# Kernel optimization log

Measured on AMD Instinct MI355X. Metric: run time of the kernel, lower is better.

Reference implementation:

```python
import jax, jax.numpy as jnp
import numpy as np

V = 1024      # visible_size (channel_size)
H = 2048      # hidden_size
F = V + H     # full_size
T = 64        # timesteps
REC = 0.8     # params['lambda']


def setup_inputs() -> dict:
    key = jax.random.key(0)
    k1, k2, k3 = jax.random.split(key, 3)
    X = jax.random.normal(k1, (T, V), jnp.float32)
    # scale W so tanh does not fully saturate (fan-in scaling, like default init)
    W = jax.random.normal(k2, (F, F), jnp.float32) / np.float32(np.sqrt(F))
    b = jax.random.normal(k3, (F,), jnp.float32) * 0.01
    # Lambda: visible block = REC, hidden block = 1, diagonal of visible block = 1
    lam = jnp.concatenate(
        [jnp.full((V, V), REC, jnp.float32), jnp.ones((V, H), jnp.float32)], axis=1
    )
    lam = lam.at[jnp.arange(V), jnp.arange(V)].set(1.0)
    return {"X": X, "W": W, "b": b, "lam": lam}


def reference(X, W, b, lam):
    v = lam.shape[0]           # visible size
    one_minus_lam_vis = 1.0 - lam[:, :v]  # zero outside visible block anyway

    def step(carry, x_t):
        R, _ = carry
        WR = R @ W.T + b                      # [V, F] Linear applied row-wise
        U = lam * WR                          # gated recurrent part
        # I has x_t broadcast across rows in the visible block, zeros elsewhere
        U = U.at[:, :v].add(one_minus_lam_vis * x_t[None, :])
        R_next = jnp.tanh(U)                  # phi = torch.tanh
        return (R_next, U), None

    R0 = jnp.zeros((v, W.shape[0]), X.dtype)
    (_, U_last), _ = jax.lax.scan(step, (R0, R0), X)
    # torch.diag(U[:, :visible]) -> diagonal entries, shape [V]
    idx = jnp.arange(v)
    return U_last[idx, idx]
```

## Files before the change

### kernel.cpp

```cpp
#include <hip/hip_runtime.h>
#include <math.h>

#define V 1024
#define H 2048
#define F 3072
#define T 64
#define REC 0.8f

#define BM 64
#define BN 96
#define KT16 (F / 16)
#define NSS  (KT16 / 4)


typedef _Float16 half8 __attribute__((ext_vector_type(8)));
typedef float floatx16 __attribute__((ext_vector_type(16)));

__device__ __forceinline__ void gld16(const void* g, void* l) {
    __builtin_amdgcn_global_load_lds(
        (const __attribute__((address_space(1))) void*)g,
        (__attribute__((address_space(3))) void*)l, 16, 0, 0);
}

__device__ __forceinline__ float fast_tanh(float u) {
    float e = __expf(2.f * u);
    return 1.f - 2.f * __builtin_amdgcn_rcpf(e + 1.f);
}

__global__ __launch_bounds__(256)
void conv_w_fm(const float* __restrict__ W, _Float16* __restrict__ Wfm) {
    const int ct = blockIdx.y;
    const int ix = blockIdx.x * 256 + threadIdx.x;
    const int kt = ix / 192;
    const int q  = ix % 192;
    const int n  = ct * 96 + ((q >> 6) & 3) * 32 + (q & 31);
    const int k0 = kt * 16 + ((q >> 5) & 1) * 8;
    const float* src = W + (size_t)n * F + k0;
    float4 v0 = *(const float4*)src;
    float4 v1 = *(const float4*)(src + 4);
    half8 o = { (_Float16)v0.x, (_Float16)v0.y, (_Float16)v0.z, (_Float16)v0.w,
                (_Float16)v1.x, (_Float16)v1.y, (_Float16)v1.z, (_Float16)v1.w };
    *(half8*)(Wfm + ((size_t)(ct * KT16 + kt) * 1536 + q * 8)) = o;
}

__global__ __launch_bounds__(256)
void init_step0(const float* __restrict__ b, const float* __restrict__ x0,
                _Float16* __restrict__ Rfm) {
    const int rt = blockIdx.y;
    const int ix = blockIdx.x * 256 + threadIdx.x;
    const int kt = ix >> 7;
    const int q  = ix & 127;
    const int gi = rt * 64 + ((q >> 6) & 1) * 32 + (q & 31);
    const int k0 = kt * 16 + ((q >> 5) & 1) * 8;
    half8 o;
    #pragma unroll
    for (int e = 0; e < 8; ++e) {
        int gj = k0 + e;
        float wr = b[gj];
        float u = (gj >= V || gi == gj) ? wr : (REC * wr + (1.f - REC) * x0[gj]);
        o[e] = (_Float16)fast_tanh(u);
    }
    *(half8*)(Rfm + ((size_t)(rt * KT16 + kt) * 1024 + q * 8)) = o;
}

__global__ __launch_bounds__(256, 2)
void frnn_step(const _Float16* __restrict__ Rin, const _Float16* __restrict__ Wfm,
               const float* __restrict__ b, const float* __restrict__ xt,
               _Float16* __restrict__ Rout, float* __restrict__ out, int is_last)
{
    __shared__ _Float16 lds[30720];

    const int tid  = threadIdx.x;
    const int lane = tid & 63;
    const int kg   = tid >> 6;
    const int bid = blockIdx.x;
    const int xcd = bid & 7;
    const int i64 = bid >> 3;
    const int ct  = xcd * 4 + (i64 >> 4);
    const int rt  = i64 & 15;
    const int row0 = rt * BM;
    const int col0 = ct * BN;
    const int lane8 = lane * 8;

    const int sq  = tid & 127;
    const int sq8 = sq * 8;
    const bool isA = (tid < 128);
    const _Float16* sgbase = isA
        ? Rin + ((size_t)rt * KT16 * 1024 + sq8)
        : Wfm + ((size_t)ct * KT16 * 1536 + sq8);

    floatx16 acc[2][3];
    #pragma unroll
    for (int i = 0; i < 2; ++i)
        #pragma unroll
        for (int j = 0; j < 3; ++j)
            #pragma unroll
            for (int r = 0; r < 16; ++r) acc[i][j][r] = 0.f;

#define STAGE(P, SS)                                                            \
  do {                                                                          \
    if (isA) {                                                                  \
        _Float16* d = &lds[(P) * 10240 + sq8];                                  \
        const _Float16* s = sgbase + (size_t)(SS) * 4096;                       \
        _Pragma("unroll")                                                       \
        for (int g = 0; g < 4; ++g) gld16(s + g * 1024, d + g * 1024);          \
    } else {                                                                    \
        _Float16* d = &lds[(P) * 10240 + 4096 + sq8];                           \
        const _Float16* s = sgbase + (size_t)(SS) * 6144;                       \
        _Pragma("unroll")                                                       \
        for (int g = 0; g < 6; ++g) gld16(s + g * 1024, d + g * 1024);          \
    }                                                                           \
  } while (0)

    STAGE(0, 0);
    asm volatile("" ::: "memory");
    STAGE(1, 1);
    asm volatile("" ::: "memory");

#define BODY(M, PR, PW)                                                         \
  {                                                                             \
    if (kg < 2) asm volatile("s_waitcnt vmcnt(4) lgkmcnt(0)" ::: "memory");     \
    else        asm volatile("s_waitcnt vmcnt(6) lgkmcnt(0)" ::: "memory");     \
    asm volatile("s_barrier" ::: "memory");                                     \
    const _Float16* sA = &lds[(PR) * 10240 + kg * 1024];                        \
    const _Float16* sB = &lds[(PR) * 10240 + 4096 + kg * 1536];                 \
    half8 a0 = *(const half8*)(sA + lane8);                                     \
    half8 a1 = *(const half8*)(sA + 512 + lane8);                               \
    half8 b0 = *(const half8*)(sB + lane8);                                     \
    half8 b1 = *(const half8*)(sB + 512 + lane8);                               \
    half8 b2 = *(const half8*)(sB + 1024 + lane8);                              \
    asm volatile("" ::: "memory");           \
    int nxt = (M) + 2; if (nxt >= NSS) nxt -= NSS;     \
    STAGE(PW, nxt);                                                             \
    acc[0][0] = __builtin_amdgcn_mfma_f32_32x32x16_f16(a0, b0, acc[0][0],0,0,0);\
    acc[0][1] = __builtin_amdgcn_mfma_f32_32x32x16_f16(a0, b1, acc[0][1],0,0,0);\
    acc[0][2] = __builtin_amdgcn_mfma_f32_32x32x16_f16(a0, b2, acc[0][2],0,0,0);\
    acc[1][0] = __builtin_amdgcn_mfma_f32_32x32x16_f16(a1, b0, acc[1][0],0,0,0);\
    acc[1][1] = __builtin_amdgcn_mfma_f32_32x32x16_f16(a1, b1, acc[1][1],0,0,0);\
    acc[1][2] = __builtin_amdgcn_mfma_f32_32x32x16_f16(a1, b2, acc[1][2],0,0,0);\
  }

    #pragma unroll 1
    for (int m3 = 0; m3 < NSS / 3; ++m3) {
        const int M = m3 * 3;
        BODY(M,     0, 2)
        BODY(M + 1, 1, 0)
        BODY(M + 2, 2, 1)
    }
#undef BODY
#undef STAGE

    asm volatile("s_waitcnt vmcnt(0) lgkmcnt(0)\n\ts_barrier" ::: "memory");

    const int m32 = lane & 31, hh = lane >> 5;
    float b_r[3], x_r[3];
    if (kg == 0) {
        #pragma unroll
        for (int j = 0; j < 3; ++j) {
            int gj = col0 + j * 32 + m32;
            b_r[j] = b[gj];
            x_r[j] = (gj < V) ? xt[gj] : 0.f;
        }
    }

    float* red = (float*)lds;
    #pragma unroll 1
    for (int w = 1; w < 4; ++w) {
        if (kg == w) {
            #pragma unroll
            for (int i = 0; i < 2; ++i)
                #pragma unroll
                for (int j = 0; j < 3; ++j)
                    #pragma unroll
                    for (int q4 = 0; q4 < 4; ++q4) {
                        float4 v = { acc[i][j][4*q4],   acc[i][j][4*q4+1],
                                     acc[i][j][4*q4+2], acc[i][j][4*q4+3] };
                        *(float4*)(red + ((i*3 + j)*4 + q4) * 256 + lane * 4) = v;
                    }
        }
        __syncthreads();
        if (kg == 0) {
            #pragma unroll
            for (int i = 0; i < 2; ++i)
                #pragma unroll
                for (int j = 0; j < 3; ++j)
                    #pragma unroll
                    for (int q4 = 0; q4 < 4; ++q4) {
                        float4 v = *(const float4*)(red + ((i*3 + j)*4 + q4) * 256 + lane * 4);
                        acc[i][j][4*q4]   += v.x; acc[i][j][4*q4+1] += v.y;
                        acc[i][j][4*q4+2] += v.z; acc[i][j][4*q4+3] += v.w;
                    }
        }
        __syncthreads();
    }

    if (kg == 0) {
        #pragma unroll
        for (int i = 0; i < 2; ++i) {
            #pragma unroll
            for (int j = 0; j < 3; ++j) {
                const int gj = col0 + j * 32 + m32;
                const int kt = gj >> 4;
                const int h2 = (gj >> 3) & 1;
                const int e  = gj & 7;
                _Float16* tb = Rout + ((size_t)(rt * KT16 + kt) * 1024
                                       + (i * 64 + h2 * 32) * 8 + e);
                const float bj = b_r[j];
                const float xj = x_r[j];
                const bool vis = (gj < V);
                #pragma unroll
                for (int r = 0; r < 16; ++r) {
                    const int mrow = 4 * hh + (r & 3) + 8 * (r >> 2);
                    const int gi = row0 + i * 32 + mrow;
                    float wr = acc[i][j][r] + bj;
                    float u = (!vis || gi == gj) ? wr : (REC * wr + (1.f - REC) * xj);
                    tb[mrow * 8] = (_Float16)fast_tanh(u);
                    if (is_last && gi == gj) out[gi] = u;
                }
            }
        }
    }
}

extern "C" void kernel_launch(void* const* d_in, const int* in_sizes, int n_in,
                              void* d_out, int out_size, void* d_ws, size_t ws_size,
                              hipStream_t stream) {
    const float* X = (const float*)d_in[0];
    const float* W = (const float*)d_in[1];
    const float* b = (const float*)d_in[2];
    float* out = (float*)d_out;

    _Float16* Wfm = (_Float16*)d_ws;
    _Float16* Ra  = Wfm + (size_t)F * F;
    _Float16* Rb  = Ra + (size_t)V * F;

    conv_w_fm<<<dim3(144, 32), 256, 0, stream>>>(W, Wfm);
    init_step0<<<dim3(96, 16), 256, 0, stream>>>(b, X, Ra);

    for (int t = 1; t < T; ++t) {
        _Float16* Rin  = (t & 1) ? Ra : Rb;
        _Float16* Rout = (t & 1) ? Rb : Ra;
        frnn_step<<<dim3(512), 256, 0, stream>>>(Rin, Wfm, b, X + (size_t)t * V,
                                                 Rout, out, t == T - 1);
    }
}
```

Before: 2.112 ms.

## Double row tile to 128 with 512-thread blocks and 4-stage LDS pipeline

Doubles the per-block row tile from 64 to 128 rows, using 8 waves per block (2 row-halves times 4 k-groups), so each staged W tile is reused across twice as many rows. The grid is halved to 256 blocks, the R fragment layout is changed to match, and the LDS pipeline goes from 3 to 4 buffers, prefetching 3 stages ahead, with a scheduling barrier before the MFMAs. This cuts W global and LDS traffic per output element. In exchange it uses more LDS per block and occupancy may drop, and 256 blocks may underfill the GPU.

```diff
diff --git a/kernel.cpp b/kernel.cpp
--- a/kernel.cpp
+++ b/kernel.cpp
@@ -7,7 +7,7 @@
 #define T 64
 #define REC 0.8f
 
-#define BM 64
+#define BM 128
 #define BN 96
 #define KT16 (F / 16)
 #define NSS  (KT16 / 4)
@@ -48,9 +48,9 @@
                 _Float16* __restrict__ Rfm) {
     const int rt = blockIdx.y;
     const int ix = blockIdx.x * 256 + threadIdx.x;
-    const int kt = ix >> 7;
-    const int q  = ix & 127;
-    const int gi = rt * 64 + ((q >> 6) & 1) * 32 + (q & 31);
+    const int kt = ix >> 8;
+    const int q  = ix & 255;
+    const int gi = rt * 128 + ((q >> 6) & 3) * 32 + (q & 31);
     const int k0 = kt * 16 + ((q >> 5) & 1) * 8;
     half8 o;
     #pragma unroll
@@ -60,33 +60,35 @@
         float u = (gj >= V || gi == gj) ? wr : (REC * wr + (1.f - REC) * x0[gj]);
         o[e] = (_Float16)fast_tanh(u);
     }
-    *(half8*)(Rfm + ((size_t)(rt * KT16 + kt) * 1024 + q * 8)) = o;
-}
-
-__global__ __launch_bounds__(256, 2)
+    *(half8*)(Rfm + ((size_t)(rt * KT16 + kt) * 2048 + q * 8)) = o;
+}
+
+__global__ __launch_bounds__(512, 2)
 void frnn_step(const _Float16* __restrict__ Rin, const _Float16* __restrict__ Wfm,
                const float* __restrict__ b, const float* __restrict__ xt,
                _Float16* __restrict__ Rout, float* __restrict__ out, int is_last)
 {
-    __shared__ _Float16 lds[30720];
+    __shared__ _Float16 lds[57344];
 
     const int tid  = threadIdx.x;
     const int lane = tid & 63;
-    const int kg   = tid >> 6;
+    const int wid  = tid >> 6;
+    const int sp   = wid & 1;
+    const int kg   = wid >> 1;
     const int bid = blockIdx.x;
     const int xcd = bid & 7;
-    const int i64 = bid >> 3;
-    const int ct  = xcd * 4 + (i64 >> 4);
-    const int rt  = i64 & 15;
+    const int idx = bid >> 3;
+    const int ct  = xcd * 4 + (idx & 3);
+    const int rt  = idx >> 2;
     const int row0 = rt * BM;
     const int col0 = ct * BN;
     const int lane8 = lane * 8;
 
-    const int sq  = tid & 127;
+    const int sq  = tid & 255;
     const int sq8 = sq * 8;
-    const bool isA = (tid < 128);
+    const bool isA = (tid < 256);
     const _Float16* sgbase = isA
-        ? Rin + ((size_t)rt * KT16 * 1024 + sq8)
+        ? Rin + ((size_t)rt * KT16 * 2048 + sq8)
         : Wfm + ((size_t)ct * KT16 * 1536 + sq8);
 
     floatx16 acc[2][3];
@@ -100,15 +102,15 @@
 #define STAGE(P, SS)                                                            \
   do {                                                                          \
     if (isA) {                                                                  \
-        _Float16* d = &lds[(P) * 10240 + sq8];                                  \
-        const _Float16* s = sgbase + (size_t)(SS) * 4096;                       \
+        _Float16* d = &lds[(P) * 14336 + sq8];                                  \
+        const _Float16* s = sgbase + (size_t)(SS) * 8192;                       \
         _Pragma("unroll")                                                       \
-        for (int g = 0; g < 4; ++g) gld16(s + g * 1024, d + g * 1024);          \
+        for (int g = 0; g < 4; ++g) gld16(s + g * 2048, d + g * 2048);          \
     } else {                                                                    \
-        _Float16* d = &lds[(P) * 10240 + 4096 + sq8];                           \
+        _Float16* d = &lds[(P) * 14336 + 8192 + sq8];                           \
         const _Float16* s = sgbase + (size_t)(SS) * 6144;                       \
         _Pragma("unroll")                                                       \
-        for (int g = 0; g < 6; ++g) gld16(s + g * 1024, d + g * 1024);          \
+        for (int g = 0; g < 3; ++g) gld16(s + g * 2048, d + g * 2048);          \
     }                                                                           \
   } while (0)
 
@@ -116,22 +118,25 @@
     asm volatile("" ::: "memory");
     STAGE(1, 1);
     asm volatile("" ::: "memory");
+    STAGE(2, 2);
+    asm volatile("" ::: "memory");
 
 #define BODY(M, PR, PW)                                                         \
   {                                                                             \
-    if (kg < 2) asm volatile("s_waitcnt vmcnt(4) lgkmcnt(0)" ::: "memory");     \
-    else        asm volatile("s_waitcnt vmcnt(6) lgkmcnt(0)" ::: "memory");     \
+    if (isA) asm volatile("s_waitcnt vmcnt(8) lgkmcnt(0)" ::: "memory");        \
+    else     asm volatile("s_waitcnt vmcnt(6) lgkmcnt(0)" ::: "memory");        \
     asm volatile("s_barrier" ::: "memory");                                     \
-    const _Float16* sA = &lds[(PR) * 10240 + kg * 1024];                        \
-    const _Float16* sB = &lds[(PR) * 10240 + 4096 + kg * 1536];                 \
-    half8 a0 = *(const half8*)(sA + lane8);                                     \
-    half8 a1 = *(const half8*)(sA + 512 + lane8);                               \
+    const _Float16* sA = &lds[(PR) * 14336 + kg * 2048];                        \
+    const _Float16* sB = &lds[(PR) * 14336 + 8192 + kg * 1536];                 \
+    half8 a0 = *(const half8*)(sA + sp * 1024 + lane8);                         \
+    half8 a1 = *(const half8*)(sA + sp * 1024 + 512 + lane8);                   \
     half8 b0 = *(const half8*)(sB + lane8);                                     \
     half8 b1 = *(const half8*)(sB + 512 + lane8);                               \
     half8 b2 = *(const half8*)(sB + 1024 + lane8);                              \
-    asm volatile("" ::: "memory");           \
-    int nxt = (M) + 2; if (nxt >= NSS) nxt -= NSS;     \
+    asm volatile("" ::: "memory");         \
+    int nxt = (M) + 3; if (nxt >= NSS) nxt -= NSS;  \
     STAGE(PW, nxt);                                                             \
+    __builtin_amdgcn_sched_barrier(0);     \
     acc[0][0] = __builtin_amdgcn_mfma_f32_32x32x16_f16(a0, b0, acc[0][0],0,0,0);\
     acc[0][1] = __builtin_amdgcn_mfma_f32_32x32x16_f16(a0, b1, acc[0][1],0,0,0);\
     acc[0][2] = __builtin_amdgcn_mfma_f32_32x32x16_f16(a0, b2, acc[0][2],0,0,0);\
@@ -141,11 +146,12 @@
   }
 
     #pragma unroll 1
-    for (int m3 = 0; m3 < NSS / 3; ++m3) {
-        const int M = m3 * 3;
-        BODY(M,     0, 2)
+    for (int m4 = 0; m4 < NSS / 4; ++m4) {
+        const int M = m4 * 4;
+        BODY(M,     0, 3)
         BODY(M + 1, 1, 0)
         BODY(M + 2, 2, 1)
+        BODY(M + 3, 3, 2)
     }
 #undef BODY
 #undef STAGE
@@ -163,7 +169,7 @@
         }
     }
 
-    float* red = (float*)lds;
+    float* red = (float*)lds + sp * 6144;
     #pragma unroll 1
     for (int w = 1; w < 4; ++w) {
         if (kg == w) {
@@ -197,21 +203,22 @@
     if (kg == 0) {
         #pragma unroll
         for (int i = 0; i < 2; ++i) {
+            const int mb = sp * 2 + i;
             #pragma unroll
             for (int j = 0; j < 3; ++j) {
                 const int gj = col0 + j * 32 + m32;
                 const int kt = gj >> 4;
                 const int h2 = (gj >> 3) & 1;
                 const int e  = gj & 7;
-                _Float16* tb = Rout + ((size_t)(rt * KT16 + kt) * 1024
-                                       + (i * 64 + h2 * 32) * 8 + e);
+                _Float16* tb = Rout + ((size_t)(rt * KT16 + kt) * 2048
+                                       + (mb * 2 + h2) * 256 + e);
                 const float bj = b_r[j];
                 const float xj = x_r[j];
                 const bool vis = (gj < V);
                 #pragma unroll
                 for (int r = 0; r < 16; ++r) {
                     const int mrow = 4 * hh + (r & 3) + 8 * (r >> 2);
-                    const int gi = row0 + i * 32 + mrow;
+                    const int gi = row0 + mb * 32 + mrow;
                     float wr = acc[i][j][r] + bj;
                     float u = (!vis || gi == gj) ? wr : (REC * wr + (1.f - REC) * xj);
                     tb[mrow * 8] = (_Float16)fast_tanh(u);
@@ -235,12 +242,12 @@
     _Float16* Rb  = Ra + (size_t)V * F;
 
     conv_w_fm<<<dim3(144, 32), 256, 0, stream>>>(W, Wfm);
-    init_step0<<<dim3(96, 16), 256, 0, stream>>>(b, X, Ra);
+    init_step0<<<dim3(192, 8), 256, 0, stream>>>(b, X, Ra);
 
     for (int t = 1; t < T; ++t) {
         _Float16* Rin  = (t & 1) ? Ra : Rb;
         _Float16* Rout = (t & 1) ? Rb : Ra;
-        frnn_step<<<dim3(512), 256, 0, stream>>>(Rin, Wfm, b, X + (size_t)t * V,
+        frnn_step<<<dim3(256), 512, 0, stream>>>(Rin, Wfm, b, X + (size_t)t * V,
                                                  Rout, out, t == T - 1);
     }
 }
```

Result: no change. 2.151 ms (+1.9%).
